# Performance work log

Hardware: AMD Instinct MI355X
Metric: run time of the kernel (lower is better)

The kernel has to match this reference:

```python
import jax, jax.numpy as jnp
import numpy as np

B, T, HID = 1, 2048, 2048
H = 16            # num_heads == num_key_value_heads
D = HID // H      # head_dim == feature_dim == 128
EPS = 1e-5


def _layer_norm(x, eps=1e-5):
    mu = jnp.mean(x, axis=-1, keepdims=True)
    var = jnp.mean((x - mu) ** 2, axis=-1, keepdims=True)
    return (x - mu) * jax.lax.rsqrt(var + eps)


def _feature_map(x, gamma, beta):
    # ReBased feature map, flatten=False (parallel mode): affine then LayerNorm
    return _layer_norm(x * gamma + beta)


def setup_inputs() -> dict:
    key = jax.random.key(0)
    ks = jax.random.split(key, 8)
    s = HID ** -0.5
    return {
        "hidden_states": jax.random.normal(ks[0], (B, T, HID), jnp.float32),
        "Wq": jax.random.normal(ks[1], (HID, HID), jnp.float32) * s,
        "Wk": jax.random.normal(ks[2], (HID, HID), jnp.float32) * s,
        "Wv": jax.random.normal(ks[3], (HID, HID), jnp.float32) * s,
        "Wo": jax.random.normal(ks[4], (HID, HID), jnp.float32) * s,
        "gamma": 1.0 + 0.1 * jax.random.normal(ks[5], (D,), jnp.float32),
        "beta": 0.1 * jax.random.normal(ks[6], (D,), jnp.float32),
    }


def reference(hidden_states, Wq, Wk, Wv, Wo, gamma, beta):
    b, t, _ = hidden_states.shape
    # projections (nn.Linear: x @ W.T), split into heads: [b, t, h, d]
    q = (hidden_states @ Wq.T).reshape(b, t, H, D)
    k = (hidden_states @ Wk.T).reshape(b, t, H, D)
    v = (hidden_states @ Wv.T).reshape(b, t, H, D)
    # ReBased feature map (no quadratic flatten in parallel mode)
    q = _feature_map(q, gamma, beta)
    k = _feature_map(k, gamma, beta)
    # parallel_rebased: scale q, quadratic score, causal mask, normalize
    q = q * (D ** -0.5)
    attn = jnp.einsum('bqhd,bkhd->bhqk', q, k) ** 2  # (q.k)^2
    mask = jnp.tril(jnp.ones((t, t), dtype=bool))
    attn = jnp.where(mask, attn, 0.0)
    o = jnp.einsum('bhqk,bkhd->bqhd', attn, v)       # [b, t, h, d]
    z = jnp.sum(attn, axis=-1)                       # [b, h, t]
    o = o / (jnp.swapaxes(z, 1, 2)[..., None] + EPS)
    o = o.reshape(b, t, H * D)
    return o @ Wo.T
```

## Files before the change

### kernel.cpp

```cpp
#include <hip/hip_runtime.h>
#include <hip/hip_bf16.h>
#include <stdint.h>

typedef __bf16 bf16;
typedef __bf16 v8bf __attribute__((ext_vector_type(8)));
typedef __bf16 v4bf __attribute__((ext_vector_type(4)));
typedef float  v4f  __attribute__((ext_vector_type(4)));

#define TSEQ   2048
#define HIDDIM 2048
#define NHEAD  16
#define HDIM   128

__device__ __forceinline__ void async16(void* lds, const void* g)
{
    __builtin_amdgcn_global_load_lds(
        (__attribute__((address_space(1))) void*)(uintptr_t)g,
        (__attribute__((address_space(3))) void*)(unsigned int)(uintptr_t)lds,
        16, 0, 0);
}

__global__ __launch_bounds__(256) void conv5(const float* __restrict__ s0, bf16* __restrict__ d0,
                                             const float* __restrict__ s1, bf16* __restrict__ d1,
                                             const float* __restrict__ s2, bf16* __restrict__ d2,
                                             const float* __restrict__ s3, bf16* __restrict__ d3,
                                             const float* __restrict__ s4, bf16* __restrict__ d4)
{
    const float* src; bf16* dst;
    switch (blockIdx.y) {
        case 0: src = s0; dst = d0; break;
        case 1: src = s1; dst = d1; break;
        case 2: src = s2; dst = d2; break;
        case 3: src = s3; dst = d3; break;
        default: src = s4; dst = d4; break;
    }
    const size_t i = ((size_t)blockIdx.x * 256 + threadIdx.x) * 8;
    const float4 a = *(const float4*)(src + i);
    const float4 b = *(const float4*)(src + i + 4);
    v8bf o;
    o[0] = (bf16)a.x; o[1] = (bf16)a.y; o[2] = (bf16)a.z; o[3] = (bf16)a.w;
    o[4] = (bf16)b.x; o[5] = (bf16)b.y; o[6] = (bf16)b.z; o[7] = (bf16)b.w;
    *(v8bf*)(dst + i) = o;
}


#define PBAR() do { __builtin_amdgcn_sched_barrier(0); __builtin_amdgcn_s_barrier(); \
                    __builtin_amdgcn_sched_barrier(0); } while (0)

#define STU(ldst, gsrc) do { \
    async16((ldst) + w*512,        (gsrc) + (size_t)(w*8 + (l>>3))*2048); \
    async16((ldst) + 4096 + w*512, (gsrc) + (size_t)(64 + w*8 + (l>>3))*2048); \
} while (0)

#define RDA(buf) do { _Pragma("unroll") \
    for (int mi_ = 0; mi_ < 4; ++mi_) { \
        const bf16* p_ = &sA[(buf)*8192 + (wm*64 + mi_*16 + lr)*64]; \
        a[mi_][0] = *(const v8bf*)(p_ + c0); \
        a[mi_][1] = *(const v8bf*)(p_ + c1); } } while (0)

#define RDB(buf, nh) do { _Pragma("unroll") \
    for (int nj_ = 0; nj_ < 2; ++nj_) { \
        const bf16* p_ = &sB[(buf)*24576 + ((nh)*128 + wn*32 + nj_*16 + lr)*64]; \
        b[nj_][0] = *(const v8bf*)(p_ + c0); \
        b[nj_][1] = *(const v8bf*)(p_ + c1); } } while (0)

#define MQ(nh) do { _Pragma("unroll") \
    for (int mi_ = 0; mi_ < 4; ++mi_) { _Pragma("unroll") \
        for (int nj_ = 0; nj_ < 2; ++nj_) { \
            acc[mi_][(nh)*2+nj_] = __builtin_amdgcn_mfma_f32_16x16x32_bf16( \
                a[mi_][0], b[nj_][0], acc[mi_][(nh)*2+nj_], 0, 0, 0); \
            acc[mi_][(nh)*2+nj_] = __builtin_amdgcn_mfma_f32_16x16x32_bf16( \
                a[mi_][1], b[nj_][1], acc[mi_][(nh)*2+nj_], 0, 0, 0); \
        } } } while (0)

#define VMC(n) asm volatile("s_waitcnt vmcnt(" #n ")" ::: "memory")

__global__ __launch_bounds__(512, 2) void gemm_qkv384(const bf16* __restrict__ A,
    const bf16* __restrict__ Wcat, bf16* __restrict__ qb, bf16* __restrict__ kb,
    bf16* __restrict__ vt, const float* __restrict__ gamma, const float* __restrict__ beta)
{
    __shared__ __attribute__((aligned(16))) bf16 sA[2*8192];
    __shared__ __attribute__((aligned(16))) bf16 sB[2*24576];
    const int n0g = blockIdx.x * 384;
    const int m0  = blockIdx.y * 128;

    const int tid = threadIdx.x, l = tid & 63, w = tid >> 6;
    const int wm = w >> 2, wn = w & 3;
    const int quad = l >> 4, lr = l & 15;
    const int scol = ((l & 7) ^ ((l >> 3) & 7)) * 8;
    const int c0 = ((quad    ) ^ (lr & 7)) * 8;
    const int c1 = ((quad + 4) ^ (lr & 7)) * 8;

    const bf16* Ag = A    + (size_t)m0  * 2048 + scol;
    const bf16* Bg = Wcat + (size_t)n0g * 2048 + scol;

    v4f  acc[4][6] = {};
    v8bf a[4][2], b[2][2];

    STU(&sA[0],           Ag);
    STU(&sB[0],           Bg);
    STU(&sB[8192],        Bg + (size_t)128*2048);
    STU(&sB[16384],       Bg + (size_t)256*2048);
    STU(&sA[8192],        Ag + 64);
    STU(&sB[24576],       Bg + 64);
    STU(&sB[24576+8192],  Bg + (size_t)128*2048 + 64);
    VMC(10);
    __builtin_amdgcn_s_barrier();
    __builtin_amdgcn_sched_barrier(0);

#pragma unroll 1
    for (int it = 0; it < 16; ++it) {
        const int k1 =  it*128 + 64;
        const int k2 = (it*128 + 128) & 2047;
        const int k3 = (it*128 + 192) & 2047;

        RDA(0); RDB(0, 0);
        STU(&sB[24576+16384], Bg + (size_t)256*2048 + k1);
        PBAR(); __builtin_amdgcn_s_setprio(1); MQ(0); __builtin_amdgcn_s_setprio(0);
        VMC(10); PBAR();
        RDB(0, 1);
        STU(&sA[0], Ag + k2);
        STU(&sB[0], Bg + k2);
        PBAR(); __builtin_amdgcn_s_setprio(1); MQ(1); __builtin_amdgcn_s_setprio(0);
        VMC(12); PBAR();
        RDB(0, 2);
        STU(&sB[8192], Bg + (size_t)128*2048 + k2);
        PBAR(); __builtin_amdgcn_s_setprio(1); MQ(2); __builtin_amdgcn_s_setprio(0);
        VMC(10); PBAR();
        RDA(1); RDB(1, 0);
        STU(&sB[16384], Bg + (size_t)256*2048 + k2);
        PBAR(); __builtin_amdgcn_s_setprio(1); MQ(0); __builtin_amdgcn_s_setprio(0);
        VMC(10); PBAR();
        RDB(1, 1);
        STU(&sA[8192],  Ag + k3);
        STU(&sB[24576], Bg + k3);
        PBAR(); __builtin_amdgcn_s_setprio(1); MQ(1); __builtin_amdgcn_s_setprio(0);
        VMC(12); PBAR();
        RDB(1, 2);
        STU(&sB[24576+8192], Bg + (size_t)128*2048 + k3);
        PBAR(); __builtin_amdgcn_s_setprio(1); MQ(2); __builtin_amdgcn_s_setprio(0);
        VMC(10); PBAR();
    }
    VMC(0);
    __syncthreads();

    bf16* sT = sB;
    const int erow = tid >> 2;
    const int ecol = (tid & 3) * 32;
    float gv[32], bv[32];
#pragma unroll
    for (int i = 0; i < 8; ++i) {
        *(float4*)&gv[i*4] = *(const float4*)(gamma + ecol + i*4);
        *(float4*)&bv[i*4] = *(const float4*)(beta  + ecol + i*4);
    }

#pragma unroll
    for (int nh = 0; nh < 3; ++nh) {
        const int colg0 = n0g + nh*128;
        const int which = colg0 >> 11;
        if (which == 2) {
#pragma unroll
            for (int mi = 0; mi < 4; ++mi) {
                const int row = m0 + wm*64 + mi*16 + quad*4;
#pragma unroll
                for (int jj = 0; jj < 2; ++jj) {
                    const int c = (colg0 & 2047) + wn*32 + jj*16 + lr;
                    v4bf pk;
#pragma unroll
                    for (int r = 0; r < 4; ++r) pk[r] = (bf16)acc[mi][nh*2+jj][r];
                    *(v4bf*)(vt + (size_t)c*2048 + row) = pk;
                }
            }
        } else {
#pragma unroll
            for (int mi = 0; mi < 4; ++mi) {
                const int row = wm*64 + mi*16 + quad*4;
#pragma unroll
                for (int jj = 0; jj < 2; ++jj) {
                    const int col = wn*32 + jj*16 + lr;
#pragma unroll
                    for (int r = 0; r < 4; ++r)
                        sT[(row + r)*136 + col] = (bf16)acc[mi][nh*2+jj][r];
                }
            }
            __syncthreads();
            float x[32];
            float s = 0.f, q = 0.f;
#pragma unroll
            for (int i = 0; i < 4; ++i) {
                const v8bf v = *(const v8bf*)&sT[erow*136 + ecol + i*8];
#pragma unroll
                for (int k = 0; k < 8; ++k) {
                    const float xv = (float)v[k] * gv[i*8+k] + bv[i*8+k];
                    x[i*8+k] = xv; s += xv; q += xv*xv;
                }
            }
            s += __shfl_xor(s, 1); q += __shfl_xor(q, 1);
            s += __shfl_xor(s, 2); q += __shfl_xor(q, 2);
            const float mu = s * (1.0f/128.0f);
            float var = q * (1.0f/128.0f) - mu*mu;
            var = fmaxf(var, 0.0f);
            bf16* Cb = (which == 0) ? qb : kb;
            const float qs = (which == 0) ? 0.08838834764831845f : 1.0f;
            const float rstd = rsqrtf(var + 1e-5f) * qs;
            bf16* dst = Cb + (size_t)(m0 + erow)*2048 + (colg0 & 2047) + ecol;
#pragma unroll
            for (int i = 0; i < 4; ++i) {
                v8bf o;
#pragma unroll
                for (int k = 0; k < 8; ++k)
                    o[k] = (bf16)((x[i*8+k] - mu) * rstd);
                *(v8bf*)(dst + i*8) = o;
            }
            __syncthreads();
        }
    }
}

__global__ __launch_bounds__(256) void gemm_out(const bf16* __restrict__ A,
    const bf16* __restrict__ B, float* __restrict__ C)
{
    __shared__ __attribute__((aligned(16))) bf16 sA[128*32];
    __shared__ __attribute__((aligned(16))) bf16 sB[64*32];
    const int m0 = blockIdx.y * 128, n0 = blockIdx.x * 64;
    const int K = HIDDIM, ldc = HIDDIM;
    const int tid  = threadIdx.x;
    const int lane = tid & 63;
    const int w    = tid >> 6;
    const int wm   = w >> 1, wn = w & 1;
    const int quad = lane >> 4, lr = lane & 15;
    const int srow = lane >> 2;
    const int scol = (lane & 3) * 8;

    const bf16* gA0 = A + (size_t)(m0 + w*32 + srow) * K + scol;
    const bf16* gB0 = B + (size_t)(n0 + w*16 + srow) * K + scol;
    bf16* lA0 = &sA[w*1024];
    bf16* lB0 = &sB[w*512];

    v4f acc[4][2] = {};

    for (int kt = 0; kt < K; kt += 32) {
        __syncthreads();
        async16(lA0,       gA0 + kt);
        async16(lA0 + 512, gA0 + (size_t)16*K + kt);
        async16(lB0,       gB0 + kt);
        __syncthreads();
        v8bf a[4], b[2];
#pragma unroll
        for (int i = 0; i < 4; ++i)
            a[i] = *(const v8bf*)&sA[(wm*64 + i*16 + lr)*32 + quad*8];
#pragma unroll
        for (int j = 0; j < 2; ++j)
            b[j] = *(const v8bf*)&sB[(wn*32 + j*16 + lr)*32 + quad*8];
#pragma unroll
        for (int i = 0; i < 4; ++i)
#pragma unroll
            for (int j = 0; j < 2; ++j)
                acc[i][j] = __builtin_amdgcn_mfma_f32_16x16x32_bf16(a[i], b[j], acc[i][j], 0, 0, 0);
    }

#pragma unroll
    for (int i = 0; i < 4; ++i) {
        const int row_b = m0 + wm*64 + i*16 + quad*4;
#pragma unroll
        for (int j = 0; j < 2; ++j) {
            const int col = n0 + wn*32 + j*16 + lr;
#pragma unroll
            for (int r = 0; r < 4; ++r)
                C[(size_t)(row_b + r)*ldc + col] = acc[i][j][r];
        }
    }
}

__global__ __launch_bounds__(512, 2) void attn(const bf16* __restrict__ qb,
                                               const bf16* __restrict__ kb,
                                               const bf16* __restrict__ vt,
                                               bf16* __restrict__ ob)
{
    __shared__ __attribute__((aligned(16))) bf16 sK[2*64*136];
    __shared__ __attribute__((aligned(16))) bf16 sV[2*128*72];
    __shared__ __attribute__((aligned(16))) bf16 sS[2*64*72];
    __shared__ __attribute__((aligned(16))) float sO[64*129];
    __shared__ __attribute__((aligned(16))) float sZ[64*17];

    const int h    = blockIdx.y;
    const int pr   = blockIdx.x;
    const int tid  = threadIdx.x, lane = tid & 63;
    const int w    = tid >> 6;
    const int g    = w >> 2;
    const int ww   = w & 3;
    const int quad = lane >> 4, lr = lane & 15;
    const int rs   = tid >> 4;
    const int cs   = (tid & 15) * 8;

#pragma unroll
    for (int ti = 0; ti < 2; ++ti) {
        const int tile = ti ? pr : (31 - pr);
        const int nch  = tile + 1;

        v8bf qa[4];
        {
            const bf16* q0 = qb + (size_t)(tile*64 + ww*16 + lr)*HIDDIM + h*HDIM + quad*8;
#pragma unroll
            for (int ks = 0; ks < 4; ++ks)
                qa[ks] = *(const v8bf*)(q0 + ks*32);
        }

        v4f  o[8] = {};
        float z[4] = {0.f, 0.f, 0.f, 0.f};

        v8bf curK[4], curV[4], nxtK[4], nxtV[4];
#pragma unroll
        for (int p = 0; p < 4; ++p) {
            curK[p] = *(const v8bf*)(kb + (size_t)(rs + p*32)*HIDDIM + h*HDIM + cs);
            curV[p] = *(const v8bf*)(vt + (size_t)(h*HDIM + rs + p*32)*HIDDIM + cs);
        }

        for (int ich = 0; ich < nch; ich += 2) {
            __syncthreads();
#pragma unroll
            for (int p = 0; p < 4; ++p) {
                const int r = rs + p*32;
                *(v8bf*)&sK[(r>>6)*8704 + (r&63)*136 + cs] = curK[p];
            }
#pragma unroll
            for (int p = 0; p < 4; ++p)
                *(v8bf*)&sV[(cs>>6)*9216 + (rs + p*32)*72 + (cs & 63)] = curV[p];

            if (ich + 2 < nch) {
                const int s1 = (ich + 2) * 64;
#pragma unroll
                for (int p = 0; p < 4; ++p) {
                    nxtK[p] = *(const v8bf*)(kb + (size_t)(s1 + rs + p*32)*HIDDIM + h*HDIM + cs);
                    nxtV[p] = *(const v8bf*)(vt + (size_t)(h*HDIM + rs + p*32)*HIDDIM + s1 + cs);
                }
            }
            __syncthreads();

            const int ch = ich + g;
            if (ch < nch) {
                const bf16* sKg = &sK[g*8704];
                const bf16* sVg = &sV[g*9216];
                bf16*       sSg = &sS[g*4608];
                const bool  diag = (ch == tile);
                const int   s0   = ch * 64;

                v8bf kbf[4][4];
#pragma unroll
                for (int nj = 0; nj < 4; ++nj)
#pragma unroll
                    for (int ks = 0; ks < 4; ++ks)
                        kbf[nj][ks] = *(const v8bf*)&sKg[(nj*16 + lr)*136 + ks*32 + quad*8];
                const int row_l = ww*16 + quad*4;
                const int qg    = tile*64 + row_l;
#pragma unroll
                for (int nj = 0; nj < 4; ++nj) {
                    v4f s4 = {0.f, 0.f, 0.f, 0.f};
#pragma unroll
                    for (int ks = 0; ks < 4; ++ks)
                        s4 = __builtin_amdgcn_mfma_f32_16x16x32_bf16(qa[ks], kbf[nj][ks], s4, 0, 0, 0);
                    const int col = nj*16 + lr;
                    const int sg  = s0 + col;
#pragma unroll
                    for (int r = 0; r < 4; ++r) {
                        float val = s4[r] * s4[r];
                        if (diag && (sg > qg + r)) val = 0.0f;
                        const bf16 vb16 = (bf16)val;
                        z[r] += (float)vb16;
                        sSg[(row_l + r)*72 + col] = vb16;
                    }
                }

#pragma unroll
                for (int ks = 0; ks < 2; ++ks) {
                    const v8bf sa = *(const v8bf*)&sSg[(ww*16 + lr)*72 + ks*32 + quad*8];
#pragma unroll
                    for (int nd = 0; nd < 8; ++nd) {
                        const v8bf vbf = *(const v8bf*)&sVg[(nd*16 + lr)*72 + ks*32 + quad*8];
                        o[nd] = __builtin_amdgcn_mfma_f32_16x16x32_bf16(sa, vbf, o[nd], 0, 0, 0);
                    }
                }
            }

            if (ich + 2 < nch) {
#pragma unroll
                for (int p = 0; p < 4; ++p) { curK[p] = nxtK[p]; curV[p] = nxtV[p]; }
            }
        }

        const int row_l = ww*16 + quad*4;
        __syncthreads();
        if (g == 1) {
#pragma unroll
            for (int nd = 0; nd < 8; ++nd)
#pragma unroll
                for (int r = 0; r < 4; ++r)
                    sO[(row_l + r)*129 + nd*16 + lr] = o[nd][r];
#pragma unroll
            for (int r = 0; r < 4; ++r)
                sZ[(row_l + r)*17 + lr] = z[r];
        }
        __syncthreads();
        if (g == 0) {
#pragma unroll
            for (int nd = 0; nd < 8; ++nd)
#pragma unroll
                for (int r = 0; r < 4; ++r)
                    o[nd][r] += sO[(row_l + r)*129 + nd*16 + lr];
#pragma unroll
            for (int r = 0; r < 4; ++r) {
                float zz = z[r] + sZ[(row_l + r)*17 + lr];
                zz += __shfl_xor(zz, 1); zz += __shfl_xor(zz, 2);
                zz += __shfl_xor(zz, 4); zz += __shfl_xor(zz, 8);
                z[r] = zz + 1e-5f;
            }
            const size_t rbase = (size_t)(tile*64 + row_l)*HIDDIM + h*HDIM;
#pragma unroll
            for (int nd = 0; nd < 8; ++nd) {
                const int col = nd*16 + lr;
#pragma unroll
                for (int r = 0; r < 4; ++r)
                    ob[rbase + (size_t)r*HIDDIM + col] = (bf16)(o[nd][r] / z[r]);
            }
        }
    }
}

extern "C" void kernel_launch(void* const* d_in, const int* in_sizes, int n_in,
                              void* d_out, int out_size, void* d_ws, size_t ws_size,
                              hipStream_t stream)
{
    const float* hs    = (const float*)d_in[0];
    const float* Wq    = (const float*)d_in[1];
    const float* Wk    = (const float*)d_in[2];
    const float* Wv    = (const float*)d_in[3];
    const float* Wo    = (const float*)d_in[4];
    const float* gamma = (const float*)d_in[5];
    const float* beta  = (const float*)d_in[6];
    float* outp = (float*)d_out;

    const size_t MAT = (size_t)TSEQ * HIDDIM;

    bf16* ws   = (bf16*)d_ws;
    bf16* hs_b = ws + 0*MAT;
    bf16* ob   = hs_b;
    bf16* Wq_b = ws + 1*MAT;
    bf16* Wk_b = ws + 2*MAT;
    bf16* Wv_b = ws + 3*MAT;
    bf16* Wo_b = ws + 4*MAT;
    bf16* vt   = ws + 5*MAT;
    bf16* qb   = (bf16*)d_out;
    bf16* kb   = (bf16*)d_out + MAT;

    conv5<<<dim3(2048, 5), 256, 0, stream>>>(hs, hs_b, Wq, Wq_b, Wk, Wk_b, Wv, Wv_b, Wo, Wo_b);
    gemm_qkv384<<<dim3(16, 16), 512, 0, stream>>>(hs_b, Wq_b, qb, kb, vt, gamma, beta);
    attn<<<dim3(16, 16), 512, 0, stream>>>(qb, kb, vt, ob);
    gemm_out<<<dim3(32, 16), 256, 0, stream>>>(ob, Wo_b, outp);
}
```

Before: 260.3 us.

## Rewrite output GEMM with 128x128 tiles, multi-buffered LDS pipeline and swizzle

The output projection GEMM moves from 128x64 tiles with 256 threads and a synchronous single-buffer K loop to 128x128 tiles with 512 threads. It uses four LDS stages of 64-wide K slabs, XOR-swizzled to avoid bank conflicts, and overlaps global-to-LDS loads of the next slabs with MFMA on the current ones. Scheduling hints (setprio, sched_barrier) are added. This aims to hide memory latency and raise MFMA utilisation, at the cost of much more LDS per block (128KB) and fewer blocks (256) in the grid.

Result: faster. 246.4 us (-5.3%).

```diff
diff --git a/kernel.cpp b/kernel.cpp
--- a/kernel.cpp
+++ b/kernel.cpp
@@ -217,57 +217,80 @@
     }
 }
 
-__global__ __launch_bounds__(256) void gemm_out(const bf16* __restrict__ A,
+
+#define RDO(aa, bb, buf) do { _Pragma("unroll") \
+    for (int mi_ = 0; mi_ < 4; ++mi_) { \
+        const bf16* p_ = &sA[(buf)*8192 + (wm*64 + mi_*16 + lr)*64]; \
+        aa[mi_][0] = *(const v8bf*)(p_ + c0); \
+        aa[mi_][1] = *(const v8bf*)(p_ + c1); } \
+    _Pragma("unroll") \
+    for (int nj_ = 0; nj_ < 2; ++nj_) { \
+        const bf16* p_ = &sB[(buf)*8192 + (wn*32 + nj_*16 + lr)*64]; \
+        bb[nj_][0] = *(const v8bf*)(p_ + c0); \
+        bb[nj_][1] = *(const v8bf*)(p_ + c1); } } while (0)
+
+#define MQO(aa, bb) do { _Pragma("unroll") \
+    for (int mi_ = 0; mi_ < 4; ++mi_) { _Pragma("unroll") \
+        for (int nj_ = 0; nj_ < 2; ++nj_) { \
+            acc[mi_][nj_] = __builtin_amdgcn_mfma_f32_16x16x32_bf16( \
+                aa[mi_][0], bb[nj_][0], acc[mi_][nj_], 0, 0, 0); \
+            acc[mi_][nj_] = __builtin_amdgcn_mfma_f32_16x16x32_bf16( \
+                aa[mi_][1], bb[nj_][1], acc[mi_][nj_], 0, 0, 0); \
+        } } } while (0)
+
+__global__ __launch_bounds__(512, 2) void gemm_out(const bf16* __restrict__ A,
     const bf16* __restrict__ B, float* __restrict__ C)
 {
-    __shared__ __attribute__((aligned(16))) bf16 sA[128*32];
-    __shared__ __attribute__((aligned(16))) bf16 sB[64*32];
-    const int m0 = blockIdx.y * 128, n0 = blockIdx.x * 64;
-    const int K = HIDDIM, ldc = HIDDIM;
-    const int tid  = threadIdx.x;
-    const int lane = tid & 63;
-    const int w    = tid >> 6;
-    const int wm   = w >> 1, wn = w & 1;
-    const int quad = lane >> 4, lr = lane & 15;
-    const int srow = lane >> 2;
-    const int scol = (lane & 3) * 8;
-
-    const bf16* gA0 = A + (size_t)(m0 + w*32 + srow) * K + scol;
-    const bf16* gB0 = B + (size_t)(n0 + w*16 + srow) * K + scol;
-    bf16* lA0 = &sA[w*1024];
-    bf16* lB0 = &sB[w*512];
-
-    v4f acc[4][2] = {};
-
-    for (int kt = 0; kt < K; kt += 32) {
-        __syncthreads();
-        async16(lA0,       gA0 + kt);
-        async16(lA0 + 512, gA0 + (size_t)16*K + kt);
-        async16(lB0,       gB0 + kt);
-        __syncthreads();
-        v8bf a[4], b[2];
-#pragma unroll
-        for (int i = 0; i < 4; ++i)
-            a[i] = *(const v8bf*)&sA[(wm*64 + i*16 + lr)*32 + quad*8];
-#pragma unroll
-        for (int j = 0; j < 2; ++j)
-            b[j] = *(const v8bf*)&sB[(wn*32 + j*16 + lr)*32 + quad*8];
-#pragma unroll
-        for (int i = 0; i < 4; ++i)
-#pragma unroll
-            for (int j = 0; j < 2; ++j)
-                acc[i][j] = __builtin_amdgcn_mfma_f32_16x16x32_bf16(a[i], b[j], acc[i][j], 0, 0, 0);
-    }
-
-#pragma unroll
-    for (int i = 0; i < 4; ++i) {
-        const int row_b = m0 + wm*64 + i*16 + quad*4;
-#pragma unroll
-        for (int j = 0; j < 2; ++j) {
-            const int col = n0 + wn*32 + j*16 + lr;
+    __shared__ __attribute__((aligned(16))) bf16 sA[4*8192];
+    __shared__ __attribute__((aligned(16))) bf16 sB[4*8192];
+    const int m0 = blockIdx.y * 128, n0 = blockIdx.x * 128;
+    const int tid = threadIdx.x, l = tid & 63, w = tid >> 6;
+    const int wm = w >> 2, wn = w & 3;
+    const int quad = l >> 4, lr = l & 15;
+    const int scol = ((l & 7) ^ ((l >> 3) & 7)) * 8;
+    const int c0 = ((quad    ) ^ (lr & 7)) * 8;
+    const int c1 = ((quad + 4) ^ (lr & 7)) * 8;
+
+    const bf16* Ag = A + (size_t)m0 * 2048 + scol;
+    const bf16* Bg = B + (size_t)n0 * 2048 + scol;
+
+    v4f  acc[4][2] = {};
+    v8bf a0[4][2], b0[2][2], a1[4][2], b1[2][2];
+
+    STU(&sA[0],    Ag);      STU(&sB[0],    Bg);
+    STU(&sA[8192], Ag + 64); STU(&sB[8192], Bg + 64);
+    VMC(0);
+    __builtin_amdgcn_s_barrier();
+    __builtin_amdgcn_sched_barrier(0);
+
+#pragma unroll 2
+    for (int p = 0; p < 16; ++p) {
+        const int e = (p & 1) * 2;
+        const int o = 2 - e;
+        const int ks0 = ((2*p + 2) & 31) * 64;
+        const int ks1 = ((2*p + 3) & 31) * 64;
+        RDO(a0, b0, e);
+        RDO(a1, b1, e + 1);
+        STU(&sA[o*8192],       Ag + ks0);  STU(&sB[o*8192],       Bg + ks0);
+        STU(&sA[(o+1)*8192],   Ag + ks1);  STU(&sB[(o+1)*8192],   Bg + ks1);
+        PBAR();
+        __builtin_amdgcn_s_setprio(1);
+        MQO(a0, b0);
+        MQO(a1, b1);
+        __builtin_amdgcn_s_setprio(0);
+        VMC(0);
+        PBAR();
+    }
+
+#pragma unroll
+    for (int mi = 0; mi < 4; ++mi) {
+        const int row = m0 + wm*64 + mi*16 + quad*4;
+#pragma unroll
+        for (int nj = 0; nj < 2; ++nj) {
+            const int col = n0 + wn*32 + nj*16 + lr;
 #pragma unroll
             for (int r = 0; r < 4; ++r)
-                C[(size_t)(row_b + r)*ldc + col] = acc[i][j][r];
+                C[(size_t)(row + r)*HIDDIM + col] = acc[mi][nj][r];
         }
     }
 }
@@ -455,5 +478,5 @@
     conv5<<<dim3(2048, 5), 256, 0, stream>>>(hs, hs_b, Wq, Wq_b, Wk, Wk_b, Wv, Wv_b, Wo, Wo_b);
     gemm_qkv384<<<dim3(16, 16), 512, 0, stream>>>(hs_b, Wq_b, qb, kb, vt, gamma, beta);
     attn<<<dim3(16, 16), 512, 0, stream>>>(qb, kb, vt, ob);
-    gemm_out<<<dim3(32, 16), 256, 0, stream>>>(ob, Wo_b, outp);
-}
+    gemm_out<<<dim3(16, 16), 512, 0, stream>>>(ob, Wo_b, outp);
+}
```
